# Optimization experiments

Measured on AMD Instinct MI355X. Metric: run time of the kernel, lower is better.

## Reference

```python
import jax, jax.numpy as jnp
import numpy as np

D_MODEL = 768
NUM_HEADS = 12
NUM_REG = 4
EPS = 1e-5


def _layernorm(x, g, b):
    mu = jnp.mean(x, axis=-1, keepdims=True)
    var = jnp.mean(jnp.square(x - mu), axis=-1, keepdims=True)
    return (x - mu) * jax.lax.rsqrt(var + EPS) * g + b


def _make_mask(seq_len):
    # True = masked (disallowed), matching torch attn_mask bool semantics.
    r1 = 1 + NUM_REG
    mask = np.ones((seq_len, seq_len), dtype=bool)
    mask[0, :] = False                      # context token attends to all
    mask[1:r1, :] = False                   # register tokens attend to all
    mask[r1:, :r1] = False                  # (not use_input_context_token) == False
    mask[r1:, r1:] = ~np.eye(seq_len - r1, dtype=bool)  # feature tokens: self only
    return jnp.asarray(mask)


def setup_inputs() -> dict:
    key = jax.random.key(0)
    ks = jax.random.split(key, 16)
    B, C, H, W = 8, D_MODEL, 32, 32
    d = D_MODEL
    s = 0.02
    inp = {
        "x": jax.random.normal(ks[0], (B, C, H, W), jnp.float32),
        "context_token": jax.random.normal(ks[1], (B, 1, d), jnp.float32),
        "register_tokens": jax.random.normal(ks[2], (B, NUM_REG, d), jnp.float32),
        "in_proj_w": jax.random.normal(ks[3], (3 * d, d), jnp.float32) * s,
        "in_proj_b": jnp.zeros((3 * d,), jnp.float32),
        "out_w": jax.random.normal(ks[4], (d, d), jnp.float32) * s,
        "out_b": jnp.zeros((d,), jnp.float32),
        "ln1_g": jnp.ones((d,), jnp.float32),
        "ln1_b": jnp.zeros((d,), jnp.float32),
        "ln2_g": jnp.ones((d,), jnp.float32),
        "ln2_b": jnp.zeros((d,), jnp.float32),
        "w1": jax.random.normal(ks[5], (4 * d, d), jnp.float32) * s,
        "b1": jnp.zeros((4 * d,), jnp.float32),
        "w2": jax.random.normal(ks[6], (d, 4 * d), jnp.float32) * s,
        "b2": jnp.zeros((d,), jnp.float32),
    }
    return inp


def reference(x, context_token, register_tokens, in_proj_w, in_proj_b,
              out_w, out_b, ln1_g, ln1_b, ln2_g, ln2_b, w1, b1, w2, b2):
    B, C, H, W = x.shape
    d, nh = D_MODEL, NUM_HEADS
    hd = d // nh
    x_flat = x.reshape(B, C, H * W).transpose(0, 2, 1)          # [B, HW, d]
    tokens = jnp.concatenate([context_token, register_tokens], axis=1)
    xw = _layernorm(jnp.concatenate([tokens, x_flat], axis=1), ln1_g, ln1_b)  # [B, S, d]
    S = xw.shape[1]

    qkv = xw @ in_proj_w.T + in_proj_b                           # [B, S, 3d]
    q, k, v = jnp.split(qkv, 3, axis=-1)
    q = q.reshape(B, S, nh, hd).transpose(0, 2, 1, 3)            # [B, nh, S, hd]
    k = k.reshape(B, S, nh, hd).transpose(0, 2, 1, 3)
    v = v.reshape(B, S, nh, hd).transpose(0, 2, 1, 3)

    scores = jnp.einsum("bhqd,bhkd->bhqk", q, k) / jnp.sqrt(jnp.float32(hd))
    mask = _make_mask(S)
    scores = jnp.where(mask, jnp.float32(-1e9), scores)
    probs = jax.nn.softmax(scores, axis=-1)
    attn = jnp.einsum("bhqk,bhkd->bhqd", probs, v)               # [B, nh, S, hd]
    attn = attn.transpose(0, 2, 1, 3).reshape(B, S, d)
    attn = attn @ out_w.T + out_b

    h1 = attn + xw                                                # residual
    ff = _layernorm(h1, ln2_g, ln2_b)
    ff = jax.nn.gelu(ff @ w1.T + b1, approximate=False) @ w2.T + b2
    out = ff + h1                                                 # [B, S, d]

    r1 = 1 + NUM_REG
    ctx_out = out[:, 0:1, :]
    reg_out = out[:, 1:r1, :]
    feat_out = out[:, r1:, :].transpose(0, 2, 1).reshape(B, C, H, W)
    return feat_out, ctx_out, reg_out
```

## Files before the change

### kernel.cpp

```cpp
#include <hip/hip_runtime.h>
#include <math.h>
#include <stdint.h>

#define SEQ 1029
#define BATCH 8
#define M_TOT (BATCH * SEQ)
#define M_PAD 8320
#define NCHUNK 17

typedef float floatx4 __attribute__((ext_vector_type(4)));
typedef __bf16 bf16x8 __attribute__((ext_vector_type(8)));

__device__ __forceinline__ unsigned short f2bf(float f) {
  union { float f; unsigned u; } v; v.f = f;
  unsigned r = v.u + 0x7fffu + ((v.u >> 16) & 1u);
  return (unsigned short)(r >> 16);
}
__device__ __forceinline__ float bf2f(unsigned short h) {
  union { unsigned u; float f; } v; v.u = ((unsigned)h) << 16;
  return v.f;
}
__device__ __forceinline__ float bf_lo(unsigned u) { union { unsigned x; float f; } v; v.x = u << 16; return v.f; }
__device__ __forceinline__ float bf_hi(unsigned u) { union { unsigned x; float f; } v; v.x = u & 0xffff0000u; return v.f; }

__device__ __forceinline__ float wave_sum(float v) {
#pragma unroll
  for (int off = 32; off > 0; off >>= 1) v += __shfl_xor(v, off, 64);
  return v;
}
__device__ __forceinline__ float wave_max(float v) {
#pragma unroll
  for (int off = 32; off > 0; off >>= 1) v = fmaxf(v, __shfl_xor(v, off, 64));
  return v;
}

__device__ __forceinline__ float fast_gelu(float v) {
  const float ax = fabsf(v) * 0.70710678118654752f;
  const float t = __builtin_amdgcn_rcpf(1.0f + 0.3275911f * ax);
  const float poly = ((((1.061405429f * t - 1.453152027f) * t + 1.421413741f) * t
                       - 0.284496736f) * t + 0.254829592f) * t;
  const float er = 1.0f - poly * __expf(-ax * ax);
  return 0.5f * v * (1.0f + copysignf(er, v));
}

__device__ __forceinline__ void gload16(const unsigned short* g, unsigned short* l) {
  __builtin_amdgcn_global_load_lds(
      (const __attribute__((address_space(1))) unsigned int*)g,
      (__attribute__((address_space(3))) unsigned int*)l, 16, 0, 0);
}

template <int C>
__device__ __forceinline__ void vwait() {
  if constexpr (C == 0) asm volatile("s_waitcnt vmcnt(0)" ::: "memory");
  else if constexpr (C == 4) asm volatile("s_waitcnt vmcnt(4)" ::: "memory");
  else asm volatile("s_waitcnt vmcnt(8)" ::: "memory");
}

#define NQ_QKV 442368
#define NQ_OUT 147456
#define NQ_W1  589824
#define NQ_W2  589824
#define NQ_PAD 8448
__global__ void convert_all(const float4* __restrict__ inw, const float4* __restrict__ outw,
                            const float4* __restrict__ w1, const float4* __restrict__ w2,
                            ushort4* __restrict__ wqkv, ushort4* __restrict__ wout,
                            ushort4* __restrict__ w1b, ushort4* __restrict__ w2b,
                            ushort4* __restrict__ xw_pad, ushort4* __restrict__ attn_pad) {
  const int i = blockIdx.x * 256 + threadIdx.x;
  const float4* src; ushort4* dst; int off;
  if (i < NQ_QKV) { src = inw; dst = wqkv; off = i; }
  else if (i < NQ_QKV + NQ_OUT) { src = outw; dst = wout; off = i - NQ_QKV; }
  else if (i < NQ_QKV + NQ_OUT + NQ_W1) { src = w1; dst = w1b; off = i - NQ_QKV - NQ_OUT; }
  else if (i < NQ_QKV + NQ_OUT + NQ_W1 + NQ_W2) { src = w2; dst = w2b; off = i - NQ_QKV - NQ_OUT - NQ_W1; }
  else {
    const int j = i - (NQ_QKV + NQ_OUT + NQ_W1 + NQ_W2);
    const ushort4 z = {0, 0, 0, 0};
    if (j < NQ_PAD) { xw_pad[j] = z; attn_pad[j] = z; }
    return;
  }
  const float4 v = src[off];
  ushort4 o;
  o.x = f2bf(v.x); o.y = f2bf(v.y); o.z = f2bf(v.z); o.w = f2bf(v.w);
  dst[off] = o;
}
#define NQ_ALL (NQ_QKV + NQ_OUT + NQ_W1 + NQ_W2 + NQ_PAD)

__global__ __launch_bounds__(256) void ln1_all(const float* __restrict__ x,
                                               const float* __restrict__ ctx,
                                               const float* __restrict__ regs,
                                               const float* __restrict__ g,
                                               const float* __restrict__ bta,
                                               unsigned short* __restrict__ xw) {
  __shared__ float tile[768 * 17];
  const int b = blockIdx.y;
  const int t = threadIdx.x;
  const int wave = t >> 6, lane = t & 63;

  if (blockIdx.x == 64) {
    for (int s = wave; s < 5; s += 4) {
      const float* src = (s == 0) ? (ctx + (size_t)b * 768)
                                  : (regs + ((size_t)b * 4 + (s - 1)) * 768);
      float vals[12], sm = 0.f, ss = 0.f;
#pragma unroll
      for (int i = 0; i < 12; i++) {
        const float v = src[lane + 64 * i];
        vals[i] = v; sm += v; ss += v * v;
      }
      sm = wave_sum(sm); ss = wave_sum(ss);
      const float mu = sm * (1.0f / 768.0f);
      const float var = ss * (1.0f / 768.0f) - mu * mu;
      const float rs = rsqrtf(var + 1e-5f);
      unsigned short* orow = xw + (size_t)(b * SEQ + s) * 768;
#pragma unroll
      for (int i = 0; i < 12; i++) {
        const int c = lane + 64 * i;
        orow[c] = f2bf((vals[i] - mu) * rs * g[c] + bta[c]);
      }
    }
    return;
  }

  const int hw0 = blockIdx.x * 16;
  const float* xb = x + (size_t)b * 768 * 1024;
  const int cl = t >> 4, hl = t & 15;
  for (int it = 0; it < 48; it++) {
    const int c = it * 16 + cl;
    tile[c * 17 + hl] = xb[(size_t)c * 1024 + hw0 + hl];
  }
  __syncthreads();
  for (int tk = wave; tk < 16; tk += 4) {
    float vals[12], s = 0.f, ss = 0.f;
#pragma unroll
    for (int i = 0; i < 12; i++) {
      const float v = tile[(lane + 64 * i) * 17 + tk];
      vals[i] = v; s += v; ss += v * v;
    }
    s = wave_sum(s); ss = wave_sum(ss);
    const float mu = s * (1.0f / 768.0f);
    const float var = ss * (1.0f / 768.0f) - mu * mu;
    const float rs = rsqrtf(var + 1e-5f);
    const int row = b * SEQ + 5 + hw0 + tk;
    unsigned short* orow = xw + (size_t)row * 768;
#pragma unroll
    for (int i = 0; i < 12; i++) {
      const int c = lane + 64 * i;
      orow[c] = f2bf((vals[i] - mu) * rs * g[c] + bta[c]);
    }
  }
}

#define BM 128
#define BN 128
#define BK 32

template <int EPI, int K, int N, int NBUF>
__global__ __launch_bounds__(256, NBUF == 2 ? 4 : 2) void gemm_bt(
    const unsigned short* __restrict__ A,
    const unsigned short* __restrict__ W,
    const float* __restrict__ bias,
    const unsigned short* __restrict__ residb,
    const float* __restrict__ residf,
    float* __restrict__ outf,
    unsigned short* __restrict__ outb) {
  __shared__ alignas(16) unsigned short As[NBUF][BM * BK];
  __shared__ alignas(16) unsigned short Ws[NBUF][BN * BK];
  const int t = threadIdx.x;
  const int wave = t >> 6, lane = t & 63;
  const int quad = lane >> 4, l16 = lane & 15;
  const int wm = (wave & 1) * 64, wn = (wave >> 1) * 64;

  constexpr int GX = N / BN;
  constexpr int NWG = GX * (M_PAD / BM);
  constexpr int Q8 = NWG / 8, R8 = NWG % 8;
  const int flat = blockIdx.y * GX + blockIdx.x;
  const int xcd = flat & 7, idx = flat >> 3;
  const int wgid = (xcd < R8 ? xcd * (Q8 + 1) : R8 * (Q8 + 1) + (xcd - R8) * Q8) + idx;
  const int tileM = (wgid / GX) * BM;
  const int tileN = (wgid % GX) * BN;

  const int rl = lane >> 2;
  const int kc8 = ((lane & 3) ^ ((rl >> 1) & 3)) * 8;
  const unsigned short* Ag = A + (size_t)(tileM + wave * 16 + rl) * K;
  const unsigned short* Wg = W + (size_t)(tileN + wave * 16 + rl) * K;
  const int ldst = wave * 512 + lane * 8;

  const int koff = ((quad ^ ((l16 >> 1) & 3)) * 8);

  const floatx4 zero4 = {0.f, 0.f, 0.f, 0.f};
  floatx4 acc[4][4];
#pragma unroll
  for (int i = 0; i < 4; i++)
#pragma unroll
    for (int j = 0; j < 4; j++) acc[i][j] = zero4;

  auto dma = [&](int k0, int buf) {
    gload16(Ag + k0 + kc8, &As[buf][0] + ldst);
    gload16(Ag + (size_t)64 * K + k0 + kc8, &As[buf][0] + ldst + 2048);
    gload16(Wg + k0 + kc8, &Ws[buf][0] + ldst);
    gload16(Wg + (size_t)64 * K + k0 + kc8, &Ws[buf][0] + ldst + 2048);
  };
  auto compute = [&](int buf) {
    bf16x8 af[4], wf[4];
#pragma unroll
    for (int i = 0; i < 4; i++)
      af[i] = *(const bf16x8*)(&As[buf][0] + (wm + i * 16 + l16) * BK + koff);
#pragma unroll
    for (int j = 0; j < 4; j++)
      wf[j] = *(const bf16x8*)(&Ws[buf][0] + (wn + j * 16 + l16) * BK + koff);
#pragma unroll
    for (int i = 0; i < 4; i++)
#pragma unroll
      for (int j = 0; j < 4; j++)
        acc[i][j] = __builtin_amdgcn_mfma_f32_16x16x32_bf16(af[i], wf[j], acc[i][j], 0, 0, 0);
  };

  constexpr int NSTEP = K / BK;
  constexpr int PF = NBUF - 1;

#pragma unroll
  for (int p = 0; p < PF; ++p) dma(p * BK, p);

  int cb = 0, db = PF % NBUF;
#pragma unroll 1
  for (int i = 0; i < NSTEP - PF; ++i) {
    vwait<4 * (NBUF - 2)>();
    __builtin_amdgcn_s_barrier();
    __builtin_amdgcn_sched_barrier(0);
    dma((i + PF) * BK, db);
    db = (db + 1 == NBUF) ? 0 : db + 1;
    compute(cb);
    cb = (cb + 1 == NBUF) ? 0 : cb + 1;
  }
  if constexpr (NBUF == 4) {
    vwait<8>(); __builtin_amdgcn_s_barrier(); __builtin_amdgcn_sched_barrier(0);
    compute(cb); cb = (cb + 1 == NBUF) ? 0 : cb + 1;
    vwait<4>(); __builtin_amdgcn_s_barrier(); __builtin_amdgcn_sched_barrier(0);
    compute(cb); cb = (cb + 1 == NBUF) ? 0 : cb + 1;
  }
  vwait<0>(); __builtin_amdgcn_s_barrier(); __builtin_amdgcn_sched_barrier(0);
  compute(cb);

#pragma unroll
  for (int i = 0; i < 4; i++) {
    const int mbase = tileM + wm + i * 16 + quad * 4;
#pragma unroll
    for (int j = 0; j < 4; j++) {
      const int n = tileN + wn + j * 16 + l16;
      const float bv = bias[n];
#pragma unroll
      for (int r = 0; r < 4; r++) {
        const size_t idx2 = (size_t)(mbase + r) * N + n;
        float v = acc[i][j][r] + bv;
        if constexpr (EPI == 0) {
          outb[idx2] = f2bf(v);
        } else if constexpr (EPI == 1) {
          outf[idx2] = v + bf2f(residb[idx2]);
        } else {
          outb[idx2] = f2bf(fast_gelu(v));
        }
      }
    }
  }
}

__global__ __launch_bounds__(256, 2) void gemm_ff2scat(
    const unsigned short* __restrict__ A,
    const unsigned short* __restrict__ W,
    const float* __restrict__ bias,
    const float* __restrict__ residf,
    float* __restrict__ dout) {
  constexpr int K = 3072, N = 768, NBUF = 4;
  __shared__ union {
    struct {
      alignas(16) unsigned short As[NBUF][BM * BK];
      alignas(16) unsigned short Ws[NBUF][BN * BK];
    } ring;
    float tr[128][133];
  } sm;
  const int t = threadIdx.x;
  const int wave = t >> 6, lane = t & 63;
  const int quad = lane >> 4, l16 = lane & 15;
  const int wm = (wave & 1) * 64, wn = (wave >> 1) * 64;

  constexpr int GX = N / BN;
  constexpr int NWG = GX * (M_PAD / BM);
  constexpr int Q8 = NWG / 8, R8 = NWG % 8;
  const int flat = blockIdx.y * GX + blockIdx.x;
  const int xcd = flat & 7, idx = flat >> 3;
  const int wgid = (xcd < R8 ? xcd * (Q8 + 1) : R8 * (Q8 + 1) + (xcd - R8) * Q8) + idx;
  const int tileM = (wgid / GX) * BM;
  const int tileN = (wgid % GX) * BN;

  const int rl = lane >> 2;
  const int kc8 = ((lane & 3) ^ ((rl >> 1) & 3)) * 8;
  const unsigned short* Ag = A + (size_t)(tileM + wave * 16 + rl) * K;
  const unsigned short* Wg = W + (size_t)(tileN + wave * 16 + rl) * K;
  const int ldst = wave * 512 + lane * 8;
  const int koff = ((quad ^ ((l16 >> 1) & 3)) * 8);

  const floatx4 zero4 = {0.f, 0.f, 0.f, 0.f};
  floatx4 acc[4][4];
#pragma unroll
  for (int i = 0; i < 4; i++)
#pragma unroll
    for (int j = 0; j < 4; j++) acc[i][j] = zero4;

  auto dma = [&](int k0, int buf) {
    gload16(Ag + k0 + kc8, &sm.ring.As[buf][0] + ldst);
    gload16(Ag + (size_t)64 * K + k0 + kc8, &sm.ring.As[buf][0] + ldst + 2048);
    gload16(Wg + k0 + kc8, &sm.ring.Ws[buf][0] + ldst);
    gload16(Wg + (size_t)64 * K + k0 + kc8, &sm.ring.Ws[buf][0] + ldst + 2048);
  };
  auto compute = [&](int buf) {
    bf16x8 af[4], wf[4];
#pragma unroll
    for (int i = 0; i < 4; i++)
      af[i] = *(const bf16x8*)(&sm.ring.As[buf][0] + (wm + i * 16 + l16) * BK + koff);
#pragma unroll
    for (int j = 0; j < 4; j++)
      wf[j] = *(const bf16x8*)(&sm.ring.Ws[buf][0] + (wn + j * 16 + l16) * BK + koff);
#pragma unroll
    for (int i = 0; i < 4; i++)
#pragma unroll
      for (int j = 0; j < 4; j++)
        acc[i][j] = __builtin_amdgcn_mfma_f32_16x16x32_bf16(af[i], wf[j], acc[i][j], 0, 0, 0);
  };

  constexpr int NSTEP = K / BK;
  constexpr int PF = NBUF - 1;
#pragma unroll
  for (int p = 0; p < PF; ++p) dma(p * BK, p);

  int cb = 0, db = PF % NBUF;
#pragma unroll 1
  for (int i = 0; i < NSTEP - PF; ++i) {
    vwait<8>();
    __builtin_amdgcn_s_barrier();
    __builtin_amdgcn_sched_barrier(0);
    dma((i + PF) * BK, db);
    db = (db + 1 == NBUF) ? 0 : db + 1;
    compute(cb);
    cb = (cb + 1 == NBUF) ? 0 : cb + 1;
  }
  vwait<8>(); __builtin_amdgcn_s_barrier(); __builtin_amdgcn_sched_barrier(0);
  compute(cb); cb = (cb + 1 == NBUF) ? 0 : cb + 1;
  vwait<4>(); __builtin_amdgcn_s_barrier(); __builtin_amdgcn_sched_barrier(0);
  compute(cb); cb = (cb + 1 == NBUF) ? 0 : cb + 1;
  vwait<0>(); __builtin_amdgcn_s_barrier(); __builtin_amdgcn_sched_barrier(0);
  compute(cb);

  __syncthreads();
#pragma unroll
  for (int i = 0; i < 4; i++) {
    const int mb = wm + i * 16 + quad * 4;
#pragma unroll
    for (int j = 0; j < 4; j++) {
      const int n_loc = wn + j * 16 + l16;
      const float bv = bias[tileN + n_loc];
#pragma unroll
      for (int r = 0; r < 4; r++) {
        const int m_loc = mb + r;
        const float v = acc[i][j][r] + bv +
                        residf[(size_t)(tileM + m_loc) * N + tileN + n_loc];
        sm.tr[m_loc][n_loc] = v;
      }
    }
  }
  __syncthreads();

  const int b0 = tileM / SEQ;
  const int bnd = (b0 + 1) * SEQ - tileM;
#pragma unroll
  for (int rh = 0; rh < 2; rh++) {
    const int row_loc = rh * 64 + lane;
    const int row = tileM + row_loc;
    const int bb = b0 + (row_loc >= bnd ? 1 : 0);
    const int s = row - bb * SEQ;
    const bool ok = row < M_TOT;
    for (int cc = 0; cc < 32; cc++) {
      const int c_loc = wave * 32 + cc;
      const int c = tileN + c_loc;
      const float v = sm.tr[row_loc][c_loc];
      if (ok) {
        if (s >= 5)
          dout[(size_t)bb * 786432 + (size_t)c * 1024 + (s - 5)] = v;
        else if (s == 0)
          dout[6291456 + (size_t)bb * 768 + c] = v;
        else
          dout[6297600 + ((size_t)bb * 4 + (s - 1)) * 768 + c] = v;
      }
    }
  }
}

__global__ __launch_bounds__(256) void attn_all(const unsigned short* __restrict__ qkv,
                                                unsigned short* __restrict__ attn,
                                                float* __restrict__ part) {
  __shared__ float kk[5][64];
  __shared__ float vv[5][64];
  __shared__ float sc[5][64];
  __shared__ float mArr[5], lArr[5];
  __shared__ float og[4][320];
  const int h = blockIdx.y, b = blockIdx.z;
  const int t = threadIdx.x;
  const size_t base = (size_t)b * SEQ;
  const int wave = t >> 6, lane = t & 63;

  if (blockIdx.x < 256) {
    for (int i = t; i < 320; i += 256) {
      const int j = i >> 6, dd = i & 63;
      const size_t rb = (base + j) * 2304 + (size_t)h * 64 + dd;
      kk[j][dd] = bf2f(qkv[rb + 768]);
      vv[j][dd] = bf2f(qkv[rb + 1536]);
    }
    __syncthreads();
    const int s = 5 + blockIdx.x * 4 + wave;
    const size_t row = (base + s) * 2304 + (size_t)h * 64;
    const float q = bf2f(qkv[row + lane]);
    const float kself = bf2f(qkv[row + 768 + lane]);
    const float vself = bf2f(qkv[row + 1536 + lane]);
    float scr[6];
#pragma unroll
    for (int j = 0; j < 5; j++) scr[j] = wave_sum(q * kk[j][lane]) * 0.125f;
    scr[5] = wave_sum(q * kself) * 0.125f;
    float mx = scr[0];
#pragma unroll
    for (int j = 1; j < 6; j++) mx = fmaxf(mx, scr[j]);
    float den = 0.f, e[6];
#pragma unroll
    for (int j = 0; j < 6; j++) { e[j] = expf(scr[j] - mx); den += e[j]; }
    const float inv = 1.0f / den;
    float o = 0.f;
#pragma unroll
    for (int j = 0; j < 5; j++) o += e[j] * vv[j][lane];
    o += e[5] * vself;
    attn[(base + s) * 768 + (size_t)h * 64 + lane] = f2bf(o * inv);
    return;
  }

  const int c = blockIdx.x - 256;
  const int kbase = (c < 16) ? (5 + 64 * c) : 0;
  const int nvalid = (c < 16) ? 64 : 5;

  for (int i = t; i < 320; i += 256)
    kk[i >> 6][i & 63] = bf2f(qkv[(base + (i >> 6)) * 2304 + (size_t)h * 64 + (i & 63)]);
  __syncthreads();

  const int keyloc = t >> 2, dc = t & 3;
  const int key = kbase + keyloc;
  const unsigned short* krow = qkv + (base + key) * 2304 + 768 + (size_t)h * 64;
  const uint4 k0 = *(const uint4*)(krow + dc * 8);
  const uint4 k1 = *(const uint4*)(krow + dc * 8 + 32);
  float kf[16];
  {
    const unsigned ku[8] = {k0.x, k0.y, k0.z, k0.w, k1.x, k1.y, k1.z, k1.w};
#pragma unroll
    for (int j = 0; j < 8; j++) { kf[2 * j] = bf_lo(ku[j]); kf[2 * j + 1] = bf_hi(ku[j]); }
  }
#pragma unroll
  for (int q = 0; q < 5; q++) {
    const float* qp = kk[q];
    float d0 = 0.f;
#pragma unroll
    for (int j = 0; j < 8; j++) d0 += qp[dc * 8 + j] * kf[j];
#pragma unroll
    for (int j = 0; j < 8; j++) d0 += qp[dc * 8 + 32 + j] * kf[8 + j];
    d0 += __shfl_xor(d0, 1, 64);
    d0 += __shfl_xor(d0, 2, 64);
    if (dc == 0) sc[q][keyloc] = (keyloc < nvalid) ? d0 * 0.125f : -1e30f;
  }
  __syncthreads();

  for (int q = wave; q < 5; q += 4) {
    const float v = sc[q][lane];
    const float m = wave_max(v);
    const float e = expf(v - m);
    sc[q][lane] = e;
    const float l = wave_sum(e);
    if (lane == 0) { mArr[q] = m; lArr[q] = l; }
  }
  __syncthreads();

  const int d = t & 63, g = t >> 6;
  float o[5] = {0.f, 0.f, 0.f, 0.f, 0.f};
  for (int i = 0; i < 16; i++) {
    const int kl = g * 16 + i;
    const float v = bf2f(qkv[(base + kbase + kl) * 2304 + 1536 + (size_t)h * 64 + d]);
#pragma unroll
    for (int q = 0; q < 5; q++) o[q] += sc[q][kl] * v;
  }
#pragma unroll
  for (int q = 0; q < 5; q++) og[g][q * 64 + d] = o[q];
  __syncthreads();

  float* pw = part + (size_t)((b * 12 + h) * NCHUNK + c) * 5 * 66;
  for (int i = t; i < 320; i += 256) {
    const int q = i >> 6, dd = i & 63;
    pw[q * 66 + 2 + dd] = og[0][i] + og[1][i] + og[2][i] + og[3][i];
    if (dd == 0) { pw[q * 66] = mArr[q]; pw[q * 66 + 1] = lArr[q]; }
  }
}

__global__ __launch_bounds__(64) void attn_comb(const float* __restrict__ part,
                                                unsigned short* __restrict__ attn) {
  const int qi = blockIdx.x, h = blockIdx.y, b = blockIdx.z;
  const int d = threadIdx.x;
  float M = -3e38f, L = 0.f, o = 0.f;
  for (int c = 0; c < NCHUNK; c++) {
    const float* p = part + ((size_t)((b * 12 + h) * NCHUNK + c) * 5 + qi) * 66;
    const float mc = p[0], lc = p[1], oc = p[2 + d];
    if (mc > M) {
      const float s = expf(M - mc);
      L = L * s + lc; o = o * s + oc; M = mc;
    } else {
      const float w = expf(mc - M);
      L += lc * w; o += oc * w;
    }
  }
  attn[((size_t)b * SEQ + qi) * 768 + (size_t)h * 64 + d] = f2bf(o / L);
}

__global__ __launch_bounds__(256) void ln2_kernel(const float* __restrict__ h1,
                                                  const float* __restrict__ g,
                                                  const float* __restrict__ bta,
                                                  unsigned short* __restrict__ out) {
  const int row = blockIdx.x * 4 + (threadIdx.x >> 6);
  const int lane = threadIdx.x & 63;
  const float* r = h1 + (size_t)row * 768;
  float vals[12], sm = 0.f, ss = 0.f;
#pragma unroll
  for (int i = 0; i < 12; i++) {
    const float v = r[lane + 64 * i];
    vals[i] = v; sm += v; ss += v * v;
  }
  sm = wave_sum(sm); ss = wave_sum(ss);
  const float mu = sm * (1.0f / 768.0f);
  const float var = ss * (1.0f / 768.0f) - mu * mu;
  const float rs = rsqrtf(var + 1e-5f);
  unsigned short* orow = out + (size_t)row * 768;
#pragma unroll
  for (int i = 0; i < 12; i++) {
    const int c = lane + 64 * i;
    orow[c] = f2bf((vals[i] - mu) * rs * g[c] + bta[c]);
  }
}

extern "C" void kernel_launch(void* const* d_in, const int* in_sizes, int n_in,
                              void* d_out, int out_size, void* d_ws, size_t ws_size,
                              hipStream_t stream) {
  const float* x    = (const float*)d_in[0];
  const float* ctx  = (const float*)d_in[1];
  const float* regs = (const float*)d_in[2];
  const float* inw  = (const float*)d_in[3];
  const float* inb  = (const float*)d_in[4];
  const float* outw = (const float*)d_in[5];
  const float* outbi= (const float*)d_in[6];
  const float* ln1g = (const float*)d_in[7];
  const float* ln1b = (const float*)d_in[8];
  const float* ln2g = (const float*)d_in[9];
  const float* ln2b = (const float*)d_in[10];
  const float* w1   = (const float*)d_in[11];
  const float* b1   = (const float*)d_in[12];
  const float* w2   = (const float*)d_in[13];
  const float* b2   = (const float*)d_in[14];

  char* ws = (char*)d_ws;
  unsigned short* wqkv_b = (unsigned short*)(ws + 0);
  unsigned short* wout_b = (unsigned short*)(ws + 3538944);
  unsigned short* w1_b   = (unsigned short*)(ws + 4718592);
  unsigned short* w2_b   = (unsigned short*)(ws + 9437184);
  unsigned short* xw_b   = (unsigned short*)(ws + 14155776);
  unsigned short* ln2o_b = (unsigned short*)(ws + 26935296);
  float*          h1_f   = (float*)(ws + 39714816);
  unsigned short* qkv_b  = (unsigned short*)(ws + 65273856);
  unsigned short* attn_b = (unsigned short*)(ws + 103612416);
  unsigned short* ffm_b  = (unsigned short*)(ws + 65273856);
  float*          part_f = (float*)(ws + 14155776);
  float* dout = (float*)d_out;

  part_f = (float*)(ws + 116391936);

  convert_all<<<(NQ_ALL + 255) / 256, 256, 0, stream>>>(
      (const float4*)inw, (const float4*)outw, (const float4*)w1, (const float4*)w2,
      (ushort4*)wqkv_b, (ushort4*)wout_b, (ushort4*)w1_b, (ushort4*)w2_b,
      (ushort4*)(xw_b + (size_t)M_TOT * 768), (ushort4*)(attn_b + (size_t)M_TOT * 768));

  ln1_all<<<dim3(65, 8), 256, 0, stream>>>(x, ctx, regs, ln1g, ln1b, xw_b);

  gemm_bt<0, 768, 2304, 2><<<dim3(2304 / BN, M_PAD / BM), 256, 0, stream>>>(
      xw_b, wqkv_b, inb, nullptr, nullptr, nullptr, qkv_b);

  attn_all<<<dim3(256 + NCHUNK, 12, 8), 256, 0, stream>>>(qkv_b, attn_b, part_f);
  attn_comb<<<dim3(5, 12, 8), 64, 0, stream>>>(part_f, attn_b);

  gemm_bt<1, 768, 768, 4><<<dim3(768 / BN, M_PAD / BM), 256, 0, stream>>>(
      attn_b, wout_b, outbi, xw_b, nullptr, h1_f, nullptr);

  ln2_kernel<<<M_PAD / 4, 256, 0, stream>>>(h1_f, ln2g, ln2b, ln2o_b);

  gemm_bt<2, 768, 3072, 2><<<dim3(3072 / BN, M_PAD / BM), 256, 0, stream>>>(
      ln2o_b, w1_b, b1, nullptr, nullptr, nullptr, ffm_b);

  gemm_ff2scat<<<dim3(768 / BN, M_PAD / BM), 256, 0, stream>>>(
      ffm_b, w2_b, b2, h1_f, dout);
}
```

Before: 378.4 us.

## Use 128x256 tiles with 512 threads for QKV and FF1 GEMMs

```diff
diff --git a/kernel.cpp b/kernel.cpp
--- a/kernel.cpp
+++ b/kernel.cpp
@@ -154,7 +154,7 @@
 #define BK 32
 
 template <int EPI, int K, int N, int NBUF>
-__global__ __launch_bounds__(256, NBUF == 2 ? 4 : 2) void gemm_bt(
+__global__ __launch_bounds__(256, 2) void gemm_bt(
     const unsigned short* __restrict__ A,
     const unsigned short* __restrict__ W,
     const float* __restrict__ bias,
@@ -183,7 +183,6 @@
   const unsigned short* Ag = A + (size_t)(tileM + wave * 16 + rl) * K;
   const unsigned short* Wg = W + (size_t)(tileN + wave * 16 + rl) * K;
   const int ldst = wave * 512 + lane * 8;
-
   const int koff = ((quad ^ ((l16 >> 1) & 3)) * 8);
 
   const floatx4 zero4 = {0.f, 0.f, 0.f, 0.f};
@@ -216,7 +215,6 @@
 
   constexpr int NSTEP = K / BK;
   constexpr int PF = NBUF - 1;
-
 #pragma unroll
   for (int p = 0; p < PF; ++p) dma(p * BK, p);
 
@@ -258,6 +256,93 @@
         } else {
           outb[idx2] = f2bf(fast_gelu(v));
         }
+      }
+    }
+  }
+}
+
+template <int EPI, int K, int N>
+__global__ __launch_bounds__(512, 6) void gemm_bn256(
+    const unsigned short* __restrict__ A,
+    const unsigned short* __restrict__ W,
+    const float* __restrict__ bias,
+    unsigned short* __restrict__ outb) {
+  __shared__ alignas(16) unsigned short As[2][128 * BK];
+  __shared__ alignas(16) unsigned short Ws[2][256 * BK];
+  const int t = threadIdx.x;
+  const int wave = t >> 6, lane = t & 63;
+  const int quad = lane >> 4, l16 = lane & 15;
+  const int wm = (wave & 1) * 64, wn = (wave >> 1) * 64;
+
+  constexpr int GX = N / 256;
+  constexpr int NWG = GX * (M_PAD / BM);
+  constexpr int Q8 = NWG / 8, R8 = NWG % 8;
+  const int flat = blockIdx.y * GX + blockIdx.x;
+  const int xcd = flat & 7, idx = flat >> 3;
+  const int wgid = (xcd < R8 ? xcd * (Q8 + 1) : R8 * (Q8 + 1) + (xcd - R8) * Q8) + idx;
+  const int tileM = (wgid / GX) * BM;
+  const int tileN = (wgid % GX) * 256;
+
+  const int rl = lane >> 2;
+  const int kc8 = ((lane & 3) ^ ((rl >> 1) & 3)) * 8;
+  const unsigned short* Ag = A + (size_t)(tileM + wave * 16 + rl) * K;
+  const unsigned short* Wg = W + (size_t)(tileN + wave * 16 + rl) * K;
+  const int ldst = t * 8;
+  const int koff = ((quad ^ ((l16 >> 1) & 3)) * 8);
+
+  const floatx4 zero4 = {0.f, 0.f, 0.f, 0.f};
+  floatx4 acc[4][4];
+#pragma unroll
+  for (int i = 0; i < 4; i++)
+#pragma unroll
+    for (int j = 0; j < 4; j++) acc[i][j] = zero4;
+
+  auto dma = [&](int k0, int buf) {
+    gload16(Ag + k0 + kc8, &As[buf][0] + ldst);
+    gload16(Wg + k0 + kc8, &Ws[buf][0] + ldst);
+    gload16(Wg + (size_t)128 * K + k0 + kc8, &Ws[buf][0] + ldst + 4096);
+  };
+  auto compute = [&](int buf) {
+    bf16x8 af[4], wf[4];
+#pragma unroll
+    for (int i = 0; i < 4; i++)
+      af[i] = *(const bf16x8*)(&As[buf][0] + (wm + i * 16 + l16) * BK + koff);
+#pragma unroll
+    for (int j = 0; j < 4; j++)
+      wf[j] = *(const bf16x8*)(&Ws[buf][0] + (wn + j * 16 + l16) * BK + koff);
+#pragma unroll
+    for (int i = 0; i < 4; i++)
+#pragma unroll
+      for (int j = 0; j < 4; j++)
+        acc[i][j] = __builtin_amdgcn_mfma_f32_16x16x32_bf16(af[i], wf[j], acc[i][j], 0, 0, 0);
+  };
+
+  constexpr int NSTEP = K / BK;
+  dma(0, 0);
+#pragma unroll 1
+  for (int i = 0; i < NSTEP - 1; ++i) {
+    vwait<0>();
+    __builtin_amdgcn_s_barrier();
+    __builtin_amdgcn_sched_barrier(0);
+    dma((i + 1) * BK, (i + 1) & 1);
+    compute(i & 1);
+  }
+  vwait<0>(); __builtin_amdgcn_s_barrier(); __builtin_amdgcn_sched_barrier(0);
+  compute((NSTEP - 1) & 1);
+
+#pragma unroll
+  for (int i = 0; i < 4; i++) {
+    const int mbase = tileM + wm + i * 16 + quad * 4;
+#pragma unroll
+    for (int j = 0; j < 4; j++) {
+      const int n = tileN + wn + j * 16 + l16;
+      const float bv = bias[n];
+#pragma unroll
+      for (int r = 0; r < 4; r++) {
+        const size_t idx2 = (size_t)(mbase + r) * N + n;
+        float v = acc[i][j][r] + bv;
+        if constexpr (EPI == 0) outb[idx2] = f2bf(v);
+        else                    outb[idx2] = f2bf(fast_gelu(v));
       }
     }
   }
@@ -575,10 +660,8 @@
   unsigned short* qkv_b  = (unsigned short*)(ws + 65273856);
   unsigned short* attn_b = (unsigned short*)(ws + 103612416);
   unsigned short* ffm_b  = (unsigned short*)(ws + 65273856);
-  float*          part_f = (float*)(ws + 14155776);
+  float*          part_f = (float*)(ws + 116391936);
   float* dout = (float*)d_out;
-
-  part_f = (float*)(ws + 116391936);
 
   convert_all<<<(NQ_ALL + 255) / 256, 256, 0, stream>>>(
       (const float4*)inw, (const float4*)outw, (const float4*)w1, (const float4*)w2,
@@ -587,8 +670,8 @@
 
   ln1_all<<<dim3(65, 8), 256, 0, stream>>>(x, ctx, regs, ln1g, ln1b, xw_b);
 
-  gemm_bt<0, 768, 2304, 2><<<dim3(2304 / BN, M_PAD / BM), 256, 0, stream>>>(
-      xw_b, wqkv_b, inb, nullptr, nullptr, nullptr, qkv_b);
+  gemm_bn256<0, 768, 2304><<<dim3(2304 / 256, M_PAD / BM), 512, 0, stream>>>(
+      xw_b, wqkv_b, inb, qkv_b);
 
   attn_all<<<dim3(256 + NCHUNK, 12, 8), 256, 0, stream>>>(qkv_b, attn_b, part_f);
   attn_comb<<<dim3(5, 12, 8), 64, 0, stream>>>(part_f, attn_b);
@@ -598,8 +681,8 @@
 
   ln2_kernel<<<M_PAD / 4, 256, 0, stream>>>(h1_f, ln2g, ln2b, ln2o_b);
 
-  gemm_bt<2, 768, 3072, 2><<<dim3(3072 / BN, M_PAD / BM), 256, 0, stream>>>(
-      ln2o_b, w1_b, b1, nullptr, nullptr, nullptr, ffm_b);
+  gemm_bn256<2, 768, 3072><<<dim3(3072 / 256, M_PAD / BM), 512, 0, stream>>>(
+      ln2o_b, w1_b, b1, ffm_b);
 
   gemm_ff2scat<<<dim3(768 / BN, M_PAD / BM), 256, 0, stream>>>(
       ffm_b, w2_b, b2, h1_f, dout);
```

After: 686.3 us. 81.4% more time.
